# Kernel optimization log

Hardware: AMD Instinct MI355X
Metric: run time of the kernel (lower is better)

## Reference

```python
import jax, jax.numpy as jnp
import numpy as np

B, C, CI, H, W = 8, 1024, 512, 56, 56
BN_EPS = 1e-5


def setup_inputs() -> dict:
    key = jax.random.key(0)
    ks = jax.random.split(key, 12)
    s_in = 1.0 / np.sqrt(C)
    s_mid = 1.0 / np.sqrt(CI)
    return {
        "x1": jax.random.normal(ks[0], (B, C, H, W), jnp.float32),
        "x2": jax.random.normal(ks[1], (B, C, H, W), jnp.float32),
        "g_w": jax.random.normal(ks[2], (CI, C), jnp.float32) * s_in,
        "g_b": jax.random.normal(ks[3], (CI,), jnp.float32) * s_in,
        "theta_w": jax.random.normal(ks[4], (CI, C), jnp.float32) * s_in,
        "theta_b": jax.random.normal(ks[5], (CI,), jnp.float32) * s_in,
        "phi_w": jax.random.normal(ks[6], (CI, C), jnp.float32) * s_in,
        "phi_b": jax.random.normal(ks[7], (CI,), jnp.float32) * s_in,
        "wz_w": jax.random.normal(ks[8], (C, CI), jnp.float32) * s_mid,
        "wz_b": jax.random.normal(ks[9], (C,), jnp.float32) * s_mid,
        "bn_gamma": jax.random.normal(ks[10], (C,), jnp.float32) * 0.1 + 1.0,
        "bn_beta": jax.random.normal(ks[11], (C,), jnp.float32) * 0.1,
    }


def reference(x1, x2, g_w, g_b, theta_w, theta_b, phi_w, phi_b, wz_w, wz_b, bn_gamma, bn_beta):
    b, c, h, w = x1.shape
    n = h * w
    # flatten spatial, channels-last: (B, N, C); 1x1 conv == per-position matmul
    x1f = x1.reshape(b, c, n).transpose(0, 2, 1)
    x2f = x2.reshape(b, c, n).transpose(0, 2, 1)
    g_x = x2f @ g_w.T + g_b            # (B, N, CI)
    th = x1f @ theta_w.T + theta_b     # (B, N, CI)
    ph = x2f @ phi_w.T + phi_b         # (B, N, CI)
    f = jnp.einsum("bnd,bmd->bnm", th, ph)   # (B, N, N) affinity
    attn = jax.nn.softmax(f, axis=-1)         # embedded-gaussian
    y = jnp.einsum("bnm,bmd->bnd", attn, g_x)  # (B, N, CI)
    wy = y @ wz_w.T + wz_b             # (B, N, C)
    # BatchNorm (training mode: batch statistics over batch+spatial dims)
    mu = wy.mean(axis=(0, 1))
    var = wy.var(axis=(0, 1))
    wy = (wy - mu) * jax.lax.rsqrt(var + BN_EPS) * bn_gamma + bn_beta
    z = wy + x1f                       # residual
    return z.transpose(0, 2, 1).reshape(b, c, h, w)
```

## Files before the change

kernel.cpp:

```cpp
#include <hip/hip_runtime.h>


typedef _Float16 half8 __attribute__((ext_vector_type(8)));
typedef float floatx4 __attribute__((ext_vector_type(4)));

constexpr int B_ = 8, C_ = 1024, CI_ = 512, N_ = 3136;
constexpr int M_ = B_ * N_;
constexpr float BN_EPS = 1e-5f;

constexpr size_t XT1_OFF = 0;
constexpr size_t XT2_OFF = XT1_OFF + (size_t)M_ * C_ * 2;
constexpr size_t WTH_OFF = XT2_OFF + (size_t)M_ * C_ * 2;
constexpr size_t WPH_OFF = WTH_OFF + (size_t)CI_ * C_ * 2;
constexpr size_t WG_OFF  = WPH_OFF + (size_t)CI_ * C_ * 2;
constexpr size_t WZB_OFF = WG_OFF  + (size_t)CI_ * C_ * 2;
constexpr size_t TH_OFF  = WZB_OFF + (size_t)C_ * CI_ * 2;
constexpr size_t PH_OFF  = TH_OFF  + (size_t)M_ * CI_ * 2;
constexpr size_t GXT_OFF = PH_OFF  + (size_t)M_ * CI_ * 2;
constexpr size_t Y_OFF   = GXT_OFF + (size_t)M_ * CI_ * 2;
constexpr size_t WY_OFF  = Y_OFF   + (size_t)M_ * CI_ * 2;
constexpr size_t SSUM_OFF= WY_OFF  + (size_t)M_ * C_ * 2;
constexpr size_t SSQ_OFF = SSUM_OFF + 4096;
constexpr size_t SC_OFF  = SSQ_OFF + 4096;

__device__ __forceinline__ ushort f2h(float f) {
    _Float16 h = (_Float16)f;
    union { _Float16 h; ushort u; } v; v.h = h;
    return v.u;
}
__device__ __forceinline__ float h2f(ushort u) {
    union { ushort u; _Float16 h; } v; v.u = u;
    return (float)v.h;
}

__global__ __launch_bounds__(256) void cvtw4(const float* __restrict__ a, const float* __restrict__ b,
                                             const float* __restrict__ c, const float* __restrict__ d,
                                             ushort* oa, ushort* ob, ushort* oc, ushort* od) {
    const float* s; ushort* o;
    switch (blockIdx.y) {
        case 0: s = a; o = oa; break;
        case 1: s = b; o = ob; break;
        case 2: s = c; o = oc; break;
        default: s = d; o = od; break;
    }
    int i = (blockIdx.x * 256 + threadIdx.x) * 4;
    float4 v = *(const float4*)&s[i];
    ushort4 u; u.x = f2h(v.x); u.y = f2h(v.y); u.z = f2h(v.z); u.w = f2h(v.w);
    *(ushort4*)&o[i] = u;
}

__global__ __launch_bounds__(256) void xpose(const float* __restrict__ x, ushort* __restrict__ xt) {
    __shared__ ushort T[64 * 68];
    const int b = blockIdx.z, n0 = blockIdx.y * 64, c0 = blockIdx.x * 64;
    const int t = threadIdx.x;
    {
        const int cl = t >> 4, jb = (t & 15) * 4;
        #pragma unroll
        for (int i = 0; i < 4; ++i) {
            int c = cl + i * 16;
            float4 v = *(const float4*)&x[((size_t)b * C_ + c0 + c) * N_ + n0 + jb];
            ushort4 u; u.x = f2h(v.x); u.y = f2h(v.y); u.z = f2h(v.z); u.w = f2h(v.w);
            *(ushort4*)&T[c * 68 + jb] = u;
        }
    }
    __syncthreads();
    {
        const int nl = t >> 4, cb = (t & 15) * 4;
        #pragma unroll
        for (int i = 0; i < 4; ++i) {
            int n = nl + i * 16;
            ushort4 u;
            u.x = T[(cb + 0) * 68 + n];
            u.y = T[(cb + 1) * 68 + n];
            u.z = T[(cb + 2) * 68 + n];
            u.w = T[(cb + 3) * 68 + n];
            *(ushort4*)&xt[((size_t)b * N_ + n0 + n) * C_ + c0 + cb] = u;
        }
    }
}

template<int K, int NOUT, int MODE>
__global__ __launch_bounds__(256, 2) void gemm_bt(
    const ushort* __restrict__ A, const ushort* __restrict__ Bt,
    const float* __restrict__ bias, ushort* __restrict__ outb,
    float* __restrict__ ssum, float* __restrict__ ssq)
{
    __shared__ ushort Als[128 * 40];
    __shared__ ushort Bls[128 * 40];
    const int t = threadIdx.x;
    const int w = t >> 6, l = t & 63, quad = l >> 4, lid = l & 15;
    const int rw = w & 1, cw = w >> 1;
    const int rowbase = blockIdx.y * 128, colbase = blockIdx.x * 128;

    floatx4 acc[4][4] = {};

    for (int ks = 0; ks < K / 32; ++ks) {
        __syncthreads();
        #pragma unroll
        for (int i = 0; i < 2; ++i) {
            int idx = t + i * 256;
            int row = idx >> 2, ch = idx & 3;
            *(uint4*)&Als[row * 40 + ch * 8] =
                *(const uint4*)&A[(size_t)(rowbase + row) * K + ks * 32 + ch * 8];
            *(uint4*)&Bls[row * 40 + ch * 8] =
                *(const uint4*)&Bt[(size_t)(colbase + row) * K + ks * 32 + ch * 8];
        }
        __syncthreads();
        half8 af[4];
        #pragma unroll
        for (int rt = 0; rt < 4; ++rt)
            af[rt] = *(const half8*)&Als[(rw * 64 + rt * 16 + lid) * 40 + quad * 8];
        #pragma unroll
        for (int ct = 0; ct < 4; ++ct) {
            half8 bf = *(const half8*)&Bls[(cw * 64 + ct * 16 + lid) * 40 + quad * 8];
            #pragma unroll
            for (int rt = 0; rt < 4; ++rt)
                acc[rt][ct] = __builtin_amdgcn_mfma_f32_16x16x32_f16(af[rt], bf, acc[rt][ct], 0, 0, 0);
        }
    }

    #pragma unroll
    for (int ct = 0; ct < 4; ++ct) {
        const int col = colbase + cw * 64 + ct * 16 + lid;
        const float bv = bias[col];
        float s = 0.f, q = 0.f;
        #pragma unroll
        for (int rt = 0; rt < 4; ++rt) {
            const int row0 = rowbase + rw * 64 + rt * 16 + quad * 4;
            if constexpr (MODE == 1) {
                const int bb = row0 / N_;
                const int nn = row0 - bb * N_;
                ushort4 u;
                u.x = f2h(acc[rt][ct][0] + bv);
                u.y = f2h(acc[rt][ct][1] + bv);
                u.z = f2h(acc[rt][ct][2] + bv);
                u.w = f2h(acc[rt][ct][3] + bv);
                *(ushort4*)&outb[((size_t)bb * CI_ + col) * N_ + nn] = u;
            } else {
                #pragma unroll
                for (int r = 0; r < 4; ++r) {
                    float v = acc[rt][ct][r] + bv;
                    outb[(size_t)(row0 + r) * NOUT + col] = f2h(v);
                    if constexpr (MODE == 2) { s += v; q += v * v; }
                }
            }
        }
        if constexpr (MODE == 2) {
            s += __shfl_xor(s, 16, 64); s += __shfl_xor(s, 32, 64);
            q += __shfl_xor(q, 16, 64); q += __shfl_xor(q, 32, 64);
            if (quad == 0) {
                atomicAdd(&ssum[col], s);
                atomicAdd(&ssq[col], q);
            }
        }
    }
}

__global__ __launch_bounds__(512, 2) void attn(
    const ushort* __restrict__ TH, const ushort* __restrict__ PH,
    const ushort* __restrict__ GXT, ushort* __restrict__ Y)
{
    __shared__ ushort STR[20480];
    __shared__ float  Ss[64 * 33];
    __shared__ ushort Ps[64 * 40];
    __shared__ float  mrow[64], lrow[64], arow[64];
    __shared__ float  red[64 * 8];

    const int t = threadIdx.x;
    const int w = t >> 6, l = t & 63, quad = l >> 4, lid = l & 15;
    const int rw = w & 3;
    const int dh = w >> 2;
    const int b = blockIdx.x / 49, q = blockIdx.x % 49;
    const int n0 = q * 64;
    const int srow = t >> 3, sj = t & 7;

    half8 thr[16];
    {
        const size_t baseTH = ((size_t)b * N_ + n0 + rw * 16 + lid) * CI_;
        #pragma unroll
        for (int kc = 0; kc < 16; ++kc)
            thr[kc] = *(const half8*)&TH[baseTH + kc * 32 + quad * 8];
    }
    if (t < 64) { mrow[t] = -1e30f; lrow[t] = 0.f; }
    floatx4 acc[16] = {};

    for (int s = 0; s < N_ / 32; ++s) {
        const int m0 = s * 32;
        __syncthreads();
        {
            const size_t basePH = ((size_t)b * N_ + m0) * CI_;
            #pragma unroll
            for (int i = 0; i < 4; ++i) {
                int idx = t + i * 512;
                int row = idx >> 6, ch = idx & 63;
                *(uint4*)&STR[row * 520 + ch * 8] =
                    *(const uint4*)&PH[basePH + (size_t)row * CI_ + ch * 8];
            }
        }
        __syncthreads();
        {
            floatx4 sacc = {};
            #pragma unroll
            for (int ks = 0; ks < 16; ++ks) {
                half8 bb = *(const half8*)&STR[(dh * 16 + lid) * 520 + ks * 32 + quad * 8];
                sacc = __builtin_amdgcn_mfma_f32_16x16x32_f16(thr[ks], bb, sacc, 0, 0, 0);
            }
            const int col = dh * 16 + lid;
            #pragma unroll
            for (int r = 0; r < 4; ++r)
                Ss[(rw * 16 + quad * 4 + r) * 33 + col] = sacc[r];
        }
        __syncthreads();
        {
            const size_t baseGX = (size_t)b * CI_ * N_ + m0;
            #pragma unroll
            for (int i = 0; i < 4; ++i) {
                int idx = t + i * 512;
                int d = idx >> 2, ch = idx & 3;
                *(uint4*)&STR[d * 40 + ch * 8] =
                    *(const uint4*)&GXT[baseGX + (size_t)d * N_ + ch * 8];
            }
        }
        {
            float pm = Ss[srow * 33 + sj * 4];
            pm = fmaxf(pm, Ss[srow * 33 + sj * 4 + 1]);
            pm = fmaxf(pm, Ss[srow * 33 + sj * 4 + 2]);
            pm = fmaxf(pm, Ss[srow * 33 + sj * 4 + 3]);
            red[srow * 8 + sj] = pm;
        }
        __syncthreads();
        if (sj == 0) {
            float m_ = red[srow * 8];
            #pragma unroll
            for (int k = 1; k < 8; ++k) m_ = fmaxf(m_, red[srow * 8 + k]);
            const float mo = mrow[srow];
            const float mn = fmaxf(mo, m_);
            mrow[srow] = mn;
            arow[srow] = __expf(mo - mn);
        }
        __syncthreads();
        {
            const float mn = mrow[srow];
            float ps = 0.f;
            #pragma unroll
            for (int k = 0; k < 4; ++k) {
                float p = __expf(Ss[srow * 33 + sj * 4 + k] - mn);
                Ps[srow * 40 + sj * 4 + k] = f2h(p);
                ps += p;
            }
            red[srow * 8 + sj] = ps;
        }
        {
            float al[4];
            #pragma unroll
            for (int r = 0; r < 4; ++r) al[r] = arow[rw * 16 + quad * 4 + r];
            #pragma unroll
            for (int ctl = 0; ctl < 16; ++ctl)
                #pragma unroll
                for (int r = 0; r < 4; ++r) acc[ctl][r] *= al[r];
        }
        __syncthreads();
        if (sj == 0) {
            float sm = 0.f;
            #pragma unroll
            for (int k = 0; k < 8; ++k) sm += red[srow * 8 + k];
            lrow[srow] = lrow[srow] * arow[srow] + sm;
        }
        {
            half8 a = *(const half8*)&Ps[(rw * 16 + lid) * 40 + quad * 8];
            #pragma unroll
            for (int ctl = 0; ctl < 16; ++ctl) {
                half8 bb = *(const half8*)&STR[(dh * 256 + ctl * 16 + lid) * 40 + quad * 8];
                acc[ctl] = __builtin_amdgcn_mfma_f32_16x16x32_f16(a, bb, acc[ctl], 0, 0, 0);
            }
        }
    }
    __syncthreads();
    float inv[4];
    #pragma unroll
    for (int r = 0; r < 4; ++r) inv[r] = 1.0f / lrow[rw * 16 + quad * 4 + r];
    const size_t baseY = ((size_t)b * N_ + n0) * CI_;
    #pragma unroll
    for (int ctl = 0; ctl < 16; ++ctl) {
        const int col = dh * 256 + ctl * 16 + lid;
        #pragma unroll
        for (int r = 0; r < 4; ++r) {
            const int row = rw * 16 + quad * 4 + r;
            Y[baseY + (size_t)row * CI_ + col] = f2h(acc[ctl][r] * inv[r]);
        }
    }
}

__global__ __launch_bounds__(256) void bnfin(const float* __restrict__ ssum, const float* __restrict__ ssq,
                                             const float* __restrict__ gamma, const float* __restrict__ beta,
                                             float* __restrict__ sc) {
    const int c = blockIdx.x * 256 + threadIdx.x;
    const float inv_m = 1.0f / (float)M_;
    const float mu = ssum[c] * inv_m;
    const float var = ssq[c] * inv_m - mu * mu;
    const float s = gamma[c] * rsqrtf(var + BN_EPS);
    sc[c] = s;
    sc[C_ + c] = beta[c] - mu * s;
}

__global__ __launch_bounds__(256) void fin(const ushort* __restrict__ wy, const float* __restrict__ x1,
                                           const float* __restrict__ sc, float* __restrict__ out) {
    __shared__ float T[64 * 65];
    const int b = blockIdx.z, n0 = blockIdx.y * 64, c0 = blockIdx.x * 64;
    const int t = threadIdx.x;
    {
        const int nl = t >> 4, cb = (t & 15) * 4;
        #pragma unroll
        for (int i = 0; i < 4; ++i) {
            int n = nl + i * 16;
            ushort4 u = *(const ushort4*)&wy[((size_t)b * N_ + n0 + n) * C_ + c0 + cb];
            T[(cb + 0) * 65 + n] = h2f(u.x);
            T[(cb + 1) * 65 + n] = h2f(u.y);
            T[(cb + 2) * 65 + n] = h2f(u.z);
            T[(cb + 3) * 65 + n] = h2f(u.w);
        }
    }
    __syncthreads();
    {
        const int cl = t >> 4, nb = (t & 15) * 4;
        #pragma unroll
        for (int i = 0; i < 4; ++i) {
            int c = cl + i * 16;
            const float scale = sc[c0 + c], shift = sc[C_ + c0 + c];
            float4 xv = *(const float4*)&x1[((size_t)b * C_ + c0 + c) * N_ + n0 + nb];
            float4 o;
            o.x = T[c * 65 + nb + 0] * scale + shift + xv.x;
            o.y = T[c * 65 + nb + 1] * scale + shift + xv.y;
            o.z = T[c * 65 + nb + 2] * scale + shift + xv.z;
            o.w = T[c * 65 + nb + 3] * scale + shift + xv.w;
            *(float4*)&out[((size_t)b * C_ + c0 + c) * N_ + n0 + nb] = o;
        }
    }
}

extern "C" void kernel_launch(void* const* d_in, const int* in_sizes, int n_in,
                              void* d_out, int out_size, void* d_ws, size_t ws_size,
                              hipStream_t stream) {
    const float* x1      = (const float*)d_in[0];
    const float* x2      = (const float*)d_in[1];
    const float* g_w     = (const float*)d_in[2];
    const float* g_b     = (const float*)d_in[3];
    const float* theta_w = (const float*)d_in[4];
    const float* theta_b = (const float*)d_in[5];
    const float* phi_w   = (const float*)d_in[6];
    const float* phi_b   = (const float*)d_in[7];
    const float* wz_w    = (const float*)d_in[8];
    const float* wz_b    = (const float*)d_in[9];
    const float* bn_g    = (const float*)d_in[10];
    const float* bn_b    = (const float*)d_in[11];
    float* out = (float*)d_out;

    char* ws = (char*)d_ws;
    ushort* XT1 = (ushort*)(ws + XT1_OFF);
    ushort* XT2 = (ushort*)(ws + XT2_OFF);
    ushort* WTH = (ushort*)(ws + WTH_OFF);
    ushort* WPH = (ushort*)(ws + WPH_OFF);
    ushort* WG  = (ushort*)(ws + WG_OFF);
    ushort* WZB = (ushort*)(ws + WZB_OFF);
    ushort* THp = (ushort*)(ws + TH_OFF);
    ushort* PHp = (ushort*)(ws + PH_OFF);
    ushort* GXTp= (ushort*)(ws + GXT_OFF);
    ushort* Yp  = (ushort*)(ws + Y_OFF);
    ushort* WYp = (ushort*)(ws + WY_OFF);
    float* ssum = (float*)(ws + SSUM_OFF);
    float* ssq  = (float*)(ws + SSQ_OFF);
    float* sc   = (float*)(ws + SC_OFF);

    hipMemsetAsync(ws + SSUM_OFF, 0, 8192, stream);

    cvtw4<<<dim3(512, 4), 256, 0, stream>>>(theta_w, phi_w, g_w, wz_w, WTH, WPH, WG, WZB);
    xpose<<<dim3(16, 49, 8), 256, 0, stream>>>(x1, XT1);
    xpose<<<dim3(16, 49, 8), 256, 0, stream>>>(x2, XT2);

    gemm_bt<1024, 512, 0><<<dim3(4, 196), 256, 0, stream>>>(XT1, WTH, theta_b, THp, nullptr, nullptr);
    gemm_bt<1024, 512, 0><<<dim3(4, 196), 256, 0, stream>>>(XT2, WPH, phi_b, PHp, nullptr, nullptr);
    gemm_bt<1024, 512, 1><<<dim3(4, 196), 256, 0, stream>>>(XT2, WG, g_b, GXTp, nullptr, nullptr);

    attn<<<dim3(B_ * 49), 512, 0, stream>>>(THp, PHp, GXTp, Yp);

    gemm_bt<512, 1024, 2><<<dim3(8, 196), 256, 0, stream>>>(Yp, WZB, wz_b, WYp, ssum, ssq);
    bnfin<<<dim3(4), 256, 0, stream>>>(ssum, ssq, bn_g, bn_b, sc);
    fin<<<dim3(16, 49, 8), 256, 0, stream>>>(WYp, x1, sc, out);
}
```

Before: 1.068 ms.

## Keep attention softmax state in registers with shuffles and halve the query tile

The online softmax in the attention kernel now runs in registers. Row max and row sum are reduced with wave shuffles, and the two column-half waves exchange partial maxima and final sums through a tiny shared array. This replaces the shared score buffer and several barriers per key step. Blocks shrink to 256 threads and 32 query rows, so the grid doubles and more blocks fit per CU. The cost is that each block reloads the same key and value tiles for half as many queries, which doubles that traffic from L2.

```diff
diff --git a/kernel.cpp b/kernel.cpp
--- a/kernel.cpp
+++ b/kernel.cpp
@@ -156,23 +156,20 @@
     }
 }
 
-__global__ __launch_bounds__(512, 2) void attn(
+__global__ __launch_bounds__(256, 3) void attn(
     const ushort* __restrict__ TH, const ushort* __restrict__ PH,
     const ushort* __restrict__ GXT, ushort* __restrict__ Y)
 {
     __shared__ ushort STR[20480];
-    __shared__ float  Ss[64 * 33];
-    __shared__ ushort Ps[64 * 40];
-    __shared__ float  mrow[64], lrow[64], arow[64];
-    __shared__ float  red[64 * 8];
+    __shared__ ushort Ps[32 * 40];
+    __shared__ float  comb[64];
 
     const int t = threadIdx.x;
     const int w = t >> 6, l = t & 63, quad = l >> 4, lid = l & 15;
-    const int rw = w & 3;
-    const int dh = w >> 2;
-    const int b = blockIdx.x / 49, q = blockIdx.x % 49;
-    const int n0 = q * 64;
-    const int srow = t >> 3, sj = t & 7;
+    const int rw = w & 1;
+    const int dh = w >> 1;
+    const int b = blockIdx.x / 98, q = blockIdx.x % 98;
+    const int n0 = q * 32;
 
     half8 thr[16];
     {
@@ -181,7 +178,10 @@
         for (int kc = 0; kc < 16; ++kc)
             thr[kc] = *(const half8*)&TH[baseTH + kc * 32 + quad * 8];
     }
-    if (t < 64) { mrow[t] = -1e30f; lrow[t] = 0.f; }
+
+    float m_old[4], l_own[4];
+    #pragma unroll
+    for (int r = 0; r < 4; ++r) { m_old[r] = -1e30f; l_own[r] = 0.f; }
     floatx4 acc[16] = {};
 
     for (int s = 0; s < N_ / 32; ++s) {
@@ -190,82 +190,68 @@
         {
             const size_t basePH = ((size_t)b * N_ + m0) * CI_;
             #pragma unroll
-            for (int i = 0; i < 4; ++i) {
-                int idx = t + i * 512;
+            for (int i = 0; i < 8; ++i) {
+                int idx = t + i * 256;
                 int row = idx >> 6, ch = idx & 63;
                 *(uint4*)&STR[row * 520 + ch * 8] =
                     *(const uint4*)&PH[basePH + (size_t)row * CI_ + ch * 8];
             }
         }
         __syncthreads();
+        floatx4 sacc = {};
         {
-            floatx4 sacc = {};
             #pragma unroll
             for (int ks = 0; ks < 16; ++ks) {
                 half8 bb = *(const half8*)&STR[(dh * 16 + lid) * 520 + ks * 32 + quad * 8];
                 sacc = __builtin_amdgcn_mfma_f32_16x16x32_f16(thr[ks], bb, sacc, 0, 0, 0);
             }
-            const int col = dh * 16 + lid;
-            #pragma unroll
-            for (int r = 0; r < 4; ++r)
-                Ss[(rw * 16 + quad * 4 + r) * 33 + col] = sacc[r];
-        }
-        __syncthreads();
+        }
         {
-            const size_t baseGX = (size_t)b * CI_ * N_ + m0;
-            #pragma unroll
-            for (int i = 0; i < 4; ++i) {
-                int idx = t + i * 512;
-                int d = idx >> 2, ch = idx & 3;
-                *(uint4*)&STR[d * 40 + ch * 8] =
-                    *(const uint4*)&GXT[baseGX + (size_t)d * N_ + ch * 8];
-            }
-        }
-        {
-            float pm = Ss[srow * 33 + sj * 4];
-            pm = fmaxf(pm, Ss[srow * 33 + sj * 4 + 1]);
-            pm = fmaxf(pm, Ss[srow * 33 + sj * 4 + 2]);
-            pm = fmaxf(pm, Ss[srow * 33 + sj * 4 + 3]);
-            red[srow * 8 + sj] = pm;
-        }
-        __syncthreads();
-        if (sj == 0) {
-            float m_ = red[srow * 8];
-            #pragma unroll
-            for (int k = 1; k < 8; ++k) m_ = fmaxf(m_, red[srow * 8 + k]);
-            const float mo = mrow[srow];
-            const float mn = fmaxf(mo, m_);
-            mrow[srow] = mn;
-            arow[srow] = __expf(mo - mn);
-        }
-        __syncthreads();
-        {
-            const float mn = mrow[srow];
-            float ps = 0.f;
-            #pragma unroll
-            for (int k = 0; k < 4; ++k) {
-                float p = __expf(Ss[srow * 33 + sj * 4 + k] - mn);
-                Ps[srow * 40 + sj * 4 + k] = f2h(p);
-                ps += p;
-            }
-            red[srow * 8 + sj] = ps;
-        }
-        {
-            float al[4];
-            #pragma unroll
-            for (int r = 0; r < 4; ++r) al[r] = arow[rw * 16 + quad * 4 + r];
-            #pragma unroll
-            for (int ctl = 0; ctl < 16; ++ctl)
+            float mq[4];
+            #pragma unroll
+            for (int r = 0; r < 4; ++r) {
+                float v = sacc[r];
+                v = fmaxf(v, __shfl_xor(v, 1, 64));
+                v = fmaxf(v, __shfl_xor(v, 2, 64));
+                v = fmaxf(v, __shfl_xor(v, 4, 64));
+                v = fmaxf(v, __shfl_xor(v, 8, 64));
+                mq[r] = v;
+            }
+            if (lid == 0) {
                 #pragma unroll
-                for (int r = 0; r < 4; ++r) acc[ctl][r] *= al[r];
-        }
-        __syncthreads();
-        if (sj == 0) {
-            float sm = 0.f;
-            #pragma unroll
-            for (int k = 0; k < 8; ++k) sm += red[srow * 8 + k];
-            lrow[srow] = lrow[srow] * arow[srow] + sm;
-        }
+                for (int r = 0; r < 4; ++r)
+                    comb[dh * 32 + rw * 16 + quad * 4 + r] = mq[r];
+            }
+            __syncthreads();
+            {
+                const size_t baseGX = (size_t)b * CI_ * N_ + m0;
+                #pragma unroll
+                for (int i = 0; i < 8; ++i) {
+                    int idx = t + i * 256;
+                    int d = idx >> 2, ch = idx & 3;
+                    *(uint4*)&STR[d * 40 + ch * 8] =
+                        *(const uint4*)&GXT[baseGX + (size_t)d * N_ + ch * 8];
+                }
+            }
+            #pragma unroll
+            for (int r = 0; r < 4; ++r) {
+                const float other = comb[(1 - dh) * 32 + rw * 16 + quad * 4 + r];
+                const float stepm = fmaxf(mq[r], other);
+                const float mn = fmaxf(m_old[r], stepm);
+                const float alpha = __expf(m_old[r] - mn);
+                m_old[r] = mn;
+                float p = __expf(sacc[r] - mn);
+                Ps[(rw * 16 + quad * 4 + r) * 40 + dh * 16 + lid] = f2h(p);
+                p += __shfl_xor(p, 1, 64);
+                p += __shfl_xor(p, 2, 64);
+                p += __shfl_xor(p, 4, 64);
+                p += __shfl_xor(p, 8, 64);
+                l_own[r] = l_own[r] * alpha + p;
+                #pragma unroll
+                for (int ctl = 0; ctl < 16; ++ctl) acc[ctl][r] *= alpha;
+            }
+        }
+        __syncthreads();
         {
             half8 a = *(const half8*)&Ps[(rw * 16 + lid) * 40 + quad * 8];
             #pragma unroll
@@ -275,10 +261,18 @@
             }
         }
     }
+    if (lid == 0) {
+        #pragma unroll
+        for (int r = 0; r < 4; ++r)
+            comb[dh * 32 + rw * 16 + quad * 4 + r] = l_own[r];
+    }
     __syncthreads();
     float inv[4];
     #pragma unroll
-    for (int r = 0; r < 4; ++r) inv[r] = 1.0f / lrow[rw * 16 + quad * 4 + r];
+    for (int r = 0; r < 4; ++r) {
+        const int row = rw * 16 + quad * 4 + r;
+        inv[r] = 1.0f / (comb[row] + comb[32 + row]);
+    }
     const size_t baseY = ((size_t)b * N_ + n0) * CI_;
     #pragma unroll
     for (int ctl = 0; ctl < 16; ++ctl) {
@@ -381,7 +375,7 @@
     gemm_bt<1024, 512, 0><<<dim3(4, 196), 256, 0, stream>>>(XT2, WPH, phi_b, PHp, nullptr, nullptr);
     gemm_bt<1024, 512, 1><<<dim3(4, 196), 256, 0, stream>>>(XT2, WG, g_b, GXTp, nullptr, nullptr);
 
-    attn<<<dim3(B_ * 49), 512, 0, stream>>>(THp, PHp, GXTp, Yp);
+    attn<<<dim3(B_ * 98), 256, 0, stream>>>(THp, PHp, GXTp, Yp);
 
     gemm_bt<512, 1024, 2><<<dim3(8, 196), 256, 0, stream>>>(Yp, WZB, wz_b, WYp, ssum, ssq);
     bnfin<<<dim3(4), 256, 0, stream>>>(ssum, ssq, bn_g, bn_b, sc);
```

After: 2.184 ms. 105% more time.
